# Kernel tuning notes

Measured on AMD Instinct MI355X. Metric: run time of the kernel, lower is better.

## Reference

```python
import jax, jax.numpy as jnp
import numpy as np

DIM = 1024
NUM_HEADS = 16
HEAD_DIM = DIM // NUM_HEADS


def setup_inputs() -> dict:
    key = jax.random.key(0)
    k1, k2, k3, k4, k5 = jax.random.split(key, 5)
    B, N, C = 4, 4096, DIM
    s = 1.0 / np.sqrt(C)
    return {
        "x": jax.random.normal(k1, (B, N, C), dtype=jnp.float32),
        "W_qkv": jax.random.uniform(k2, (C, 3 * C), dtype=jnp.float32, minval=-s, maxval=s),
        "b_qkv": jax.random.uniform(k3, (3 * C,), dtype=jnp.float32, minval=-s, maxval=s),
        "W_proj": jax.random.uniform(k4, (C, C), dtype=jnp.float32, minval=-s, maxval=s),
        "b_proj": jax.random.uniform(k5, (C,), dtype=jnp.float32, minval=-s, maxval=s),
    }


def reference(x, W_qkv, b_qkv, W_proj, b_proj):
    B, N, C = x.shape
    H, D = NUM_HEADS, HEAD_DIM
    qkv = x @ W_qkv + b_qkv                      # [B,N,3C]
    qkv = qkv.reshape(B, N, 3, H, D).transpose(2, 0, 3, 1, 4)  # [3,B,H,N,D]
    q, k, v = qkv[0], qkv[1], qkv[2]
    q = jax.nn.softmax(q, axis=-1)               # softmax over head_dim
    k = jax.nn.softmax(k, axis=-2)               # softmax over sequence N
    context = jnp.einsum('bhnd,bhne->bhde', k, v)  # [B,H,D,D]
    out = jnp.einsum('bhnd,bhde->bhne', q, context)  # [B,H,N,D]
    out = out.transpose(0, 2, 1, 3).reshape(B, N, C)
    return out @ W_proj + b_proj
```

## Files before the change

### kernel.cpp

```cpp
#include <hip/hip_runtime.h>

#define BBATCH 4
#define SEQ 4096
#define CC 1024
#define HH 16
#define DD 64
#define TOKENS 16384
#define QKV3 3072

typedef __attribute__((ext_vector_type(8))) short short8;
typedef __attribute__((ext_vector_type(4))) float floatx4;

__device__ __forceinline__ unsigned short f2bf(float x) {
    unsigned int u = __float_as_uint(x);
    u += 0x7fff + ((u >> 16) & 1);
    return (unsigned short)(u >> 16);
}
__device__ __forceinline__ float bf2f(unsigned short h) {
    return __uint_as_float((unsigned int)h << 16);
}

__device__ __forceinline__ void gload_lds16(const void* g, void* l) {
    __builtin_amdgcn_global_load_lds(
        (const __attribute__((address_space(1))) unsigned int*)g,
        (__attribute__((address_space(3))) unsigned int*)l, 16, 0, 0);
}

__global__ __launch_bounds__(256) void cvt_bf16_kernel(
    const float* __restrict__ X, unsigned short* __restrict__ Y, long n4)
{
    long i = (long)blockIdx.x * 256 + threadIdx.x;
    if (i >= n4) return;
    float4 v = *reinterpret_cast<const float4*>(&X[i * 4]);
    ushort4 h;
    h.x = f2bf(v.x); h.y = f2bf(v.y); h.z = f2bf(v.z); h.w = f2bf(v.w);
    *reinterpret_cast<ushort4*>(&Y[i * 4]) = h;
}

__global__ __launch_bounds__(256) void transpose_bf16_kernel(
    const float* __restrict__ W, int K, int N, unsigned short* __restrict__ T)
{
    __shared__ unsigned short Lh[32][36];
    const int k0 = blockIdx.y * 32, n0 = blockIdx.x * 32;
    const int t = threadIdx.x;
    const int r = t >> 3, c4 = (t & 7) * 4;

    float4 w = *reinterpret_cast<const float4*>(&W[(size_t)(k0 + r) * N + n0 + c4]);
    Lh[r][c4 + 0] = f2bf(w.x);
    Lh[r][c4 + 1] = f2bf(w.y);
    Lh[r][c4 + 2] = f2bf(w.z);
    Lh[r][c4 + 3] = f2bf(w.w);
    __syncthreads();

    const int rn = t >> 3, ck = (t & 7) * 4;
    ushort4 h4;
    h4.x = Lh[ck + 0][rn]; h4.y = Lh[ck + 1][rn];
    h4.z = Lh[ck + 2][rn]; h4.w = Lh[ck + 3][rn];
    *reinterpret_cast<ushort4*>(&T[(size_t)(n0 + rn) * K + k0 + ck]) = h4;
}

template <int MODE>
__global__ __launch_bounds__(512) void gemm256_bf16_kernel(
    const unsigned short* __restrict__ A, int lda,
    const unsigned short* __restrict__ Bt, int ldb,
    const float* __restrict__ bias,
    float* __restrict__ Cf, int ldc,
    unsigned short* __restrict__ Qo, unsigned short* __restrict__ Ko,
    unsigned short* __restrict__ Vo)
{
    __shared__ unsigned short smem[65536];

    const int t = threadIdx.x;
    const int wave = t >> 6, lane = t & 63;

    const int gx = gridDim.x;
    const int nwg = gx * gridDim.y;
    const int id0 = blockIdx.y * gx + blockIdx.x;
    const int cpx = nwg >> 3;
    const int swzid = (id0 & 7) * cpx + (id0 >> 3);
    const int bx = swzid % gx, by = swzid / gx;

    const int row0 = by * 256, col0 = bx * 256;
    const int wave_m = wave >> 2, wave_n = wave & 3;

    const unsigned short* Bp = Bt;
    if (MODE == 0) Bp += ((size_t)(row0 >> 12)) << 20;

    const int fr  = lane & 15;
    const int fqb = (lane >> 4) << 4;
    const int sm  = (fr & 7) << 4;
    const int ck0 = ((0  + fqb) ^ sm) >> 1;
    const int ck1 = ((64 + fqb) ^ sm) >> 1;
    const int aRow = (wave_m * 128 + fr) * 64;
    const int bRow = (wave_n * 64 + fr) * 64;

    int srow[2], scol[2];
#pragma unroll
    for (int e = 0; e < 2; e++) {
        const int P  = (wave << 10) + (lane << 4) + (e << 13);
        const int r  = P >> 7;
        const int pc = P & 127;
        srow[e] = r;
        scol[e] = (pc ^ ((r & 7) << 4)) >> 1;
    }

    auto STAGE_PART = [&](int kt, int buf, int part) {
        const int isB = part >> 1, half = part & 1;
        const unsigned short* p = isB ? Bp : A;
        const int r0 = isB ? col0 : row0;
        const int ld = isB ? ldb : lda;
        const int ldsOff = buf * 32768 + isB * 16384 + half * 8192 + wave * 512;
#pragma unroll
        for (int e = 0; e < 2; e++)
            gload_lds16(&p[(size_t)(r0 + half * 128 + srow[e]) * ld
                           + ((kt & 15) << 6) + scol[e]],
                        &smem[ldsOff + e * 4096]);
    };

    floatx4 acc[8][4];
#pragma unroll
    for (int i = 0; i < 8; i++)
#pragma unroll
        for (int j = 0; j < 4; j++) acc[i][j] = (floatx4)0.0f;

    short8 a[4][2], bl[2][2], bh[2][2];

#define RDA(BUF, IH)                                                          \
    _Pragma("unroll") for (int ii = 0; ii < 4; ii++) {                        \
        a[ii][0] = *reinterpret_cast<const short8*>(                          \
            &smem[(BUF) * 32768 + aRow + ((IH) * 64 + ii * 16) * 64 + ck0]);  \
        a[ii][1] = *reinterpret_cast<const short8*>(                          \
            &smem[(BUF) * 32768 + aRow + ((IH) * 64 + ii * 16) * 64 + ck1]);  \
    }
#define RDB(BUF, JH, DST)                                                     \
    _Pragma("unroll") for (int jj = 0; jj < 2; jj++) {                        \
        DST[jj][0] = *reinterpret_cast<const short8*>(                        \
            &smem[(BUF) * 32768 + 16384 + bRow + ((JH) * 32 + jj * 16) * 64 + ck0]); \
        DST[jj][1] = *reinterpret_cast<const short8*>(                        \
            &smem[(BUF) * 32768 + 16384 + bRow + ((JH) * 32 + jj * 16) * 64 + ck1]); \
    }
#define MFMA_Q(IH, JH, BB)                                                    \
    __builtin_amdgcn_s_setprio(1);                                            \
    _Pragma("unroll") for (int ii = 0; ii < 4; ii++)                          \
    _Pragma("unroll") for (int jj = 0; jj < 2; jj++) {                        \
        acc[(IH)*4+ii][(JH)*2+jj] = __builtin_amdgcn_mfma_f32_16x16x32_bf16(  \
            a[ii][0], BB[jj][0], acc[(IH)*4+ii][(JH)*2+jj], 0, 0, 0);         \
        acc[(IH)*4+ii][(JH)*2+jj] = __builtin_amdgcn_mfma_f32_16x16x32_bf16(  \
            a[ii][1], BB[jj][1], acc[(IH)*4+ii][(JH)*2+jj], 0, 0, 0);         \
    }                                                                         \
    __builtin_amdgcn_s_setprio(0);
#define BARRIER __builtin_amdgcn_s_barrier()
#define WAIT_LGKM asm volatile("s_waitcnt lgkmcnt(0)" ::: "memory")
#define WAIT_VM2  asm volatile("s_waitcnt vmcnt(2)" ::: "memory")

#define KTILE(CUR, OTH, TN, TX)                                               \
    {                                                                         \
        RDA(CUR, 0); RDB(CUR, 0, bl);                                         \
        STAGE_PART(TN, OTH, 1);                                               \
        BARRIER; WAIT_LGKM; MFMA_Q(0, 0, bl); BARRIER;                        \
        RDB(CUR, 1, bh);                                                      \
        STAGE_PART(TN, OTH, 2);                                               \
        BARRIER; WAIT_LGKM; MFMA_Q(0, 1, bh); BARRIER;                        \
        RDA(CUR, 1);                                                          \
        STAGE_PART(TN, OTH, 3);                                               \
        BARRIER; WAIT_LGKM; MFMA_Q(1, 1, bh); BARRIER;                        \
        STAGE_PART(TX, CUR, 0);                                               \
        WAIT_VM2;                                                             \
        BARRIER;                                                              \
        MFMA_Q(1, 0, bl);                                                     \
        BARRIER;                                                              \
    }

    STAGE_PART(0, 0, 0); STAGE_PART(0, 0, 1);
    STAGE_PART(0, 0, 2); STAGE_PART(0, 0, 3);
    STAGE_PART(1, 1, 0);
    WAIT_VM2;
    BARRIER;

#pragma unroll 1
    for (int it = 0; it < 8; it++) {
        const int t1 = 2 * it + 1, t2 = 2 * it + 2, t3 = 2 * it + 3;
        KTILE(0, 1, t1, t2);
        KTILE(1, 0, t2, t3);
    }

#undef KTILE
#undef WAIT_VM2
#undef WAIT_LGKM
#undef BARRIER
#undef MFMA_Q
#undef RDB
#undef RDA

    const int cn = lane & 15, cq = (lane >> 4) * 4;

    if (MODE == 0) {
#pragma unroll
        for (int j = 0; j < 4; j++) {
            const int col = col0 + wave_n * 64 + j * 16 + cn;
            const float bv = bias[col];
#pragma unroll
            for (int i = 0; i < 8; i++)
#pragma unroll
                for (int r = 0; r < 4; r++) {
                    const int row = row0 + wave_m * 128 + i * 16 + cq + r;
                    Cf[(size_t)row * ldc + col] = acc[i][j][r] + bv;
                }
        }
        return;
    }

    __syncthreads();

#pragma unroll
    for (int j = 0; j < 4; j++) {
        const int colL = wave_n * 64 + j * 16 + cn;
        const float bv = bias[col0 + colL];
#pragma unroll
        for (int i = 0; i < 8; i++)
#pragma unroll
            for (int r = 0; r < 4; r++) {
                const int lr = wave_m * 128 + i * 16 + cq + r;
                smem[lr * 256 + (colL ^ ((lr & 7) << 3))] = f2bf(acc[i][j][r] + bv);
            }
    }
    __syncthreads();

    {
        unsigned short* outp = (bx < 4) ? Qo : ((bx < 8) ? Ko : Vo);
        const bool isQ = (bx < 4);
        const int R = t >> 1, half = t & 1;
        const size_t obase = (size_t)(row0 + R) * CC + (col0 & 1023) + half * 128;
        unsigned short* orow = &outp[obase];

#pragma unroll
        for (int g = 0; g < 2; g++) {
            short8 bufv[8];
            const int cbase = half * 16 + g * 8;
#pragma unroll
            for (int k = 0; k < 8; k++)
                bufv[k] = *reinterpret_cast<const short8*>(
                    &smem[R * 256 + (((cbase + k) ^ (R & 7)) << 3)]);
            if (isQ) {
                float v[64];
                float mx = -3.0e38f;
#pragma unroll
                for (int k = 0; k < 8; k++)
#pragma unroll
                    for (int e = 0; e < 8; e++) {
                        const float f = bf2f((unsigned short)bufv[k][e]);
                        v[k * 8 + e] = f;
                        mx = fmaxf(mx, f);
                    }
                float s = 0.0f;
#pragma unroll
                for (int q = 0; q < 64; q++) {
                    const float ev = __expf(v[q] - mx);
                    v[q] = ev;
                    s += ev;
                }
                const float inv = 1.0f / s;
#pragma unroll
                for (int k = 0; k < 8; k++)
#pragma unroll
                    for (int e = 0; e < 8; e++)
                        bufv[k][e] = (short)f2bf(v[k * 8 + e] * inv);
            }
#pragma unroll
            for (int k = 0; k < 8; k++)
                *reinterpret_cast<short8*>(&orow[g * 64 + k * 8]) = bufv[k];
        }
    }
}

__global__ __launch_bounds__(256) void kv_ctx_kernel(
    const unsigned short* __restrict__ Km, const unsigned short* __restrict__ Vm,
    float* __restrict__ ctx_p, float* __restrict__ csum_p)
{
    const int bh = blockIdx.x, ch = blockIdx.y;
    const int b = bh >> 4, h = bh & 15;
    const int t = threadIdx.x;

    __shared__ float Ks[32][68];
    __shared__ float Vs[32][68];
    __shared__ float cred[4][64];

    const int d0 = (t >> 4) * 4, e0 = (t & 15) * 4;
    float acc[4][4];
#pragma unroll
    for (int i = 0; i < 4; i++)
#pragma unroll
        for (int j = 0; j < 4; j++) acc[i][j] = 0.0f;
    float csacc = 0.0f;
    const int dc = t & 63, rq = (t >> 6) * 8;

    const size_t base = (size_t)(b * SEQ + ch * 256) * CC + (size_t)h * 64;

    for (int n0 = 0; n0 < 256; n0 += 32) {
        __syncthreads();
#pragma unroll
        for (int l = 0; l < 2; l++) {
            const int idx = t + l * 256;
            const int r = idx >> 4, c4 = (idx & 15) * 4;
            ushort4 kv = *reinterpret_cast<const ushort4*>(&Km[base + (size_t)(n0 + r) * CC + c4]);
            ushort4 vv = *reinterpret_cast<const ushort4*>(&Vm[base + (size_t)(n0 + r) * CC + c4]);
            float4 kf;
            kf.x = __expf(bf2f(kv.x));
            kf.y = __expf(bf2f(kv.y));
            kf.z = __expf(bf2f(kv.z));
            kf.w = __expf(bf2f(kv.w));
            float4 vf = {bf2f(vv.x), bf2f(vv.y), bf2f(vv.z), bf2f(vv.w)};
            *reinterpret_cast<float4*>(&Ks[r][c4]) = kf;
            *reinterpret_cast<float4*>(&Vs[r][c4]) = vf;
        }
        __syncthreads();

#pragma unroll
        for (int r = 0; r < 8; r++) csacc += Ks[rq + r][dc];

#pragma unroll 8
        for (int n = 0; n < 32; n++) {
            float4 a = *reinterpret_cast<const float4*>(&Ks[n][d0]);
            float4 v4 = *reinterpret_cast<const float4*>(&Vs[n][e0]);
            float a4[4] = {a.x, a.y, a.z, a.w};
            float b4[4] = {v4.x, v4.y, v4.z, v4.w};
#pragma unroll
            for (int i = 0; i < 4; i++)
#pragma unroll
                for (int j = 0; j < 4; j++)
                    acc[i][j] += a4[i] * b4[j];
        }
    }

    __syncthreads();
    cred[t >> 6][dc] = csacc;
    __syncthreads();

    const size_t pslot = (size_t)ch * 64 + bh;
    if (t < 64)
        csum_p[pslot * 64 + t] =
            cred[0][t] + cred[1][t] + cred[2][t] + cred[3][t];

    float* cp = &ctx_p[pslot * 4096];
#pragma unroll
    for (int i = 0; i < 4; i++) {
        float4 v4 = {acc[i][0], acc[i][1], acc[i][2], acc[i][3]};
        *reinterpret_cast<float4*>(&cp[(d0 + i) * 64 + e0]) = v4;
    }
}

__global__ __launch_bounds__(256) void reduce_ctx_kernel(
    const float* __restrict__ ctx_p, const float* __restrict__ csum_p,
    float* __restrict__ ctx, float* __restrict__ csum)
{
    const int bh = blockIdx.x, q = blockIdx.y;
    const int t = threadIdx.x;
#pragma unroll
    for (int e = 0; e < 4; e++) {
        const int idx = (q * 4 + e) * 256 + t;
        float s = 0.0f;
#pragma unroll
        for (int p = 0; p < 16; p++)
            s += ctx_p[((size_t)p * 64 + bh) * 4096 + idx];
        ctx[(size_t)bh * 4096 + idx] = s;
    }
    if (q == 0 && t < 64) {
        float s = 0.0f;
#pragma unroll
        for (int p = 0; p < 16; p++)
            s += csum_p[((size_t)p * 64 + bh) * 64 + t];
        csum[(size_t)bh * 64 + t] = s;
    }
}

__global__ __launch_bounds__(256) void weff_kernel(
    const float* __restrict__ ctx, const float* __restrict__ csum,
    const float* __restrict__ Wp, unsigned short* __restrict__ WeffT)
{
    const int bh = blockIdx.x, nc = blockIdx.y;
    const int b = bh >> 4, h = bh & 15;
    const int t = threadIdx.x;

    __shared__ float ctxs[64 * 64];
    __shared__ float cinvs[64];
#pragma unroll
    for (int l = 0; l < 16; l++)
        ctxs[t + l * 256] = ctx[(size_t)bh * 4096 + t + l * 256];
    if (t < 64) cinvs[t] = 1.0f / csum[(size_t)bh * 64 + t];
    __syncthreads();

    const int n = nc * 128 + (t & 127);
    const int dg = (t >> 7) * 32;

    float acc[32];
#pragma unroll
    for (int d = 0; d < 32; d++) acc[d] = 0.0f;

    for (int e = 0; e < 64; e++) {
        const float w = Wp[(size_t)(h * 64 + e) * CC + n];
#pragma unroll
        for (int d = 0; d < 32; d++)
            acc[d] += ctxs[(dg + d) * 64 + e] * w;
    }

    const size_t obase = ((size_t)b << 20) + (size_t)n * CC + h * 64 + dg;
#pragma unroll
    for (int d = 0; d < 32; d += 2) {
        ushort2 o;
        o.x = f2bf(acc[d] * cinvs[dg + d]);
        o.y = f2bf(acc[d + 1] * cinvs[dg + d + 1]);
        *reinterpret_cast<ushort2*>(&WeffT[obase + d]) = o;
    }
}

extern "C" void kernel_launch(void* const* d_in, const int* in_sizes, int n_in,
                              void* d_out, int out_size, void* d_ws, size_t ws_size,
                              hipStream_t stream)
{
    const float* x      = (const float*)d_in[0];
    const float* W_qkv  = (const float*)d_in[1];
    const float* b_qkv  = (const float*)d_in[2];
    const float* W_proj = (const float*)d_in[3];
    const float* b_proj = (const float*)d_in[4];
    float* out = (float*)d_out;

    unsigned short* Qm  = (unsigned short*)d_ws;
    unsigned short* Km  = Qm + (size_t)TOKENS * CC;
    unsigned short* Vm  = Km + (size_t)TOKENS * CC;
    unsigned short* xb  = Vm + (size_t)TOKENS * CC;
    unsigned short* wqT = xb + (size_t)TOKENS * CC;
    unsigned short* WeffT = wqT + (size_t)QKV3 * CC;
    float* ctx    = (float*)(WeffT + (size_t)BBATCH * CC * CC);
    float* csum   = ctx + (size_t)64 * 4096;
    float* ctx_p  = (float*)xb;
    float* csum_p = ctx_p + (size_t)16 * 64 * 4096;

    cvt_bf16_kernel<<<(TOKENS * CC / 4 + 255) / 256, 256, 0, stream>>>(
        x, xb, (long)TOKENS * CC / 4);
    transpose_bf16_kernel<<<dim3(QKV3 / 32, CC / 32), 256, 0, stream>>>(
        W_qkv, CC, QKV3, wqT);

    gemm256_bf16_kernel<1><<<dim3(QKV3 / 256, TOKENS / 256), 512, 0, stream>>>(
        xb, CC, wqT, CC, b_qkv, (float*)nullptr, 0, Qm, Km, Vm);

    kv_ctx_kernel<<<dim3(BBATCH * HH, 16), 256, 0, stream>>>(Km, Vm, ctx_p, csum_p);

    reduce_ctx_kernel<<<dim3(BBATCH * HH, 4), 256, 0, stream>>>(
        ctx_p, csum_p, ctx, csum);

    weff_kernel<<<dim3(BBATCH * HH, 8), 256, 0, stream>>>(ctx, csum, W_proj, WeffT);

    gemm256_bf16_kernel<0><<<dim3(CC / 256, TOKENS / 256), 512, 0, stream>>>(
        Qm, CC, WeffT, CC, b_proj, out, CC, nullptr, nullptr, nullptr);
}
```

Measured before the change: 371.3 us.

## Split output GEMM into 256x128 tile kernel and retile weff and kv_ctx loads

New measurement: 364.6 us. Within noise of the previous version (-1.8%).

```diff
diff --git a/kernel.cpp b/kernel.cpp
--- a/kernel.cpp
+++ b/kernel.cpp
@@ -59,12 +59,10 @@
     *reinterpret_cast<ushort4*>(&T[(size_t)(n0 + rn) * K + k0 + ck]) = h4;
 }
 
-template <int MODE>
-__global__ __launch_bounds__(512) void gemm256_bf16_kernel(
+__global__ __launch_bounds__(512) void gemm_qkv_kernel(
     const unsigned short* __restrict__ A, int lda,
     const unsigned short* __restrict__ Bt, int ldb,
     const float* __restrict__ bias,
-    float* __restrict__ Cf, int ldc,
     unsigned short* __restrict__ Qo, unsigned short* __restrict__ Ko,
     unsigned short* __restrict__ Vo)
 {
@@ -84,7 +82,6 @@
     const int wave_m = wave >> 2, wave_n = wave & 3;
 
     const unsigned short* Bp = Bt;
-    if (MODE == 0) Bp += ((size_t)(row0 >> 12)) << 20;
 
     const int fr  = lane & 15;
     const int fqb = (lane >> 4) << 4;
@@ -194,22 +191,6 @@
 
     const int cn = lane & 15, cq = (lane >> 4) * 4;
 
-    if (MODE == 0) {
-#pragma unroll
-        for (int j = 0; j < 4; j++) {
-            const int col = col0 + wave_n * 64 + j * 16 + cn;
-            const float bv = bias[col];
-#pragma unroll
-            for (int i = 0; i < 8; i++)
-#pragma unroll
-                for (int r = 0; r < 4; r++) {
-                    const int row = row0 + wave_m * 128 + i * 16 + cq + r;
-                    Cf[(size_t)row * ldc + col] = acc[i][j][r] + bv;
-                }
-        }
-        return;
-    }
-
     __syncthreads();
 
 #pragma unroll
@@ -273,6 +254,146 @@
     }
 }
 
+__global__ __launch_bounds__(512) void gemm_out_kernel(
+    const unsigned short* __restrict__ A, int lda,
+    const unsigned short* __restrict__ Bt, int ldb,
+    const float* __restrict__ bias,
+    float* __restrict__ Cf, int ldc)
+{
+    __shared__ unsigned short smem[49152];
+
+    const int t = threadIdx.x;
+    const int wave = t >> 6, lane = t & 63;
+
+    const int gx = gridDim.x;
+    const int nwg = gx * gridDim.y;
+    const int id0 = blockIdx.y * gx + blockIdx.x;
+    const int cpx = nwg >> 3;
+    const int swzid = (id0 & 7) * cpx + (id0 >> 3);
+    const int bx = swzid % gx, by = swzid / gx;
+
+    const int row0 = by * 256, col0 = bx * 128;
+    const int wave_m = wave >> 2, wave_n = wave & 3;
+
+    const unsigned short* Bp = Bt + (((size_t)(row0 >> 12)) << 20);
+
+    const int fr  = lane & 15;
+    const int fqb = (lane >> 4) << 4;
+    const int sm  = (fr & 7) << 4;
+    const int ck0 = ((0  + fqb) ^ sm) >> 1;
+    const int ck1 = ((64 + fqb) ^ sm) >> 1;
+    const int aRow = (wave_m * 128 + fr) * 64;
+    const int bRow = (wave_n * 32 + fr) * 64;
+
+    int srow[2], scol[2];
+#pragma unroll
+    for (int e = 0; e < 2; e++) {
+        const int P  = (wave << 10) + (lane << 4) + (e << 13);
+        const int r  = P >> 7;
+        const int pc = P & 127;
+        srow[e] = r;
+        scol[e] = (pc ^ ((r & 7) << 4)) >> 1;
+    }
+
+    auto STAGE_PART = [&](int kt, int buf, int part) {
+        const int isB = (part == 2);
+        const unsigned short* p = isB ? Bp : A;
+        const int r0 = isB ? col0 : (row0 + (part & 1) * 128);
+        const int ld = isB ? ldb : lda;
+        const int ldsOff = buf * 24576 + (isB ? 16384 : (part & 1) * 8192) + wave * 512;
+#pragma unroll
+        for (int e = 0; e < 2; e++)
+            gload_lds16(&p[(size_t)(r0 + srow[e]) * ld
+                           + ((kt & 15) << 6) + scol[e]],
+                        &smem[ldsOff + e * 4096]);
+    };
+
+    floatx4 acc[8][2];
+#pragma unroll
+    for (int i = 0; i < 8; i++)
+#pragma unroll
+        for (int j = 0; j < 2; j++) acc[i][j] = (floatx4)0.0f;
+
+    short8 a[4][2], bb[2][2];
+
+#define RDA(BUF, IH)                                                          \
+    _Pragma("unroll") for (int ii = 0; ii < 4; ii++) {                        \
+        a[ii][0] = *reinterpret_cast<const short8*>(                          \
+            &smem[(BUF) * 24576 + aRow + ((IH) * 64 + ii * 16) * 64 + ck0]);  \
+        a[ii][1] = *reinterpret_cast<const short8*>(                          \
+            &smem[(BUF) * 24576 + aRow + ((IH) * 64 + ii * 16) * 64 + ck1]);  \
+    }
+#define RDB(BUF)                                                              \
+    _Pragma("unroll") for (int jj = 0; jj < 2; jj++) {                        \
+        bb[jj][0] = *reinterpret_cast<const short8*>(                         \
+            &smem[(BUF) * 24576 + 16384 + bRow + (jj * 16) * 64 + ck0]);      \
+        bb[jj][1] = *reinterpret_cast<const short8*>(                         \
+            &smem[(BUF) * 24576 + 16384 + bRow + (jj * 16) * 64 + ck1]);      \
+    }
+#define MFMA_8(IH, J)                                                         \
+    __builtin_amdgcn_s_setprio(1);                                            \
+    _Pragma("unroll") for (int ii = 0; ii < 4; ii++) {                        \
+        acc[(IH)*4+ii][(J)] = __builtin_amdgcn_mfma_f32_16x16x32_bf16(        \
+            a[ii][0], bb[(J)][0], acc[(IH)*4+ii][(J)], 0, 0, 0);              \
+        acc[(IH)*4+ii][(J)] = __builtin_amdgcn_mfma_f32_16x16x32_bf16(        \
+            a[ii][1], bb[(J)][1], acc[(IH)*4+ii][(J)], 0, 0, 0);              \
+    }                                                                         \
+    __builtin_amdgcn_s_setprio(0);
+#define BARRIER __builtin_amdgcn_s_barrier()
+#define WAIT_LGKM asm volatile("s_waitcnt lgkmcnt(0)" ::: "memory")
+#define WAIT_VM2  asm volatile("s_waitcnt vmcnt(2)" ::: "memory")
+
+#define KTILE(CUR, OTH, TN, TX)                                               \
+    {                                                                         \
+        RDA(CUR, 0); RDB(CUR);                                                \
+        STAGE_PART(TN, OTH, 1);                                               \
+        BARRIER; WAIT_LGKM; MFMA_8(0, 0); BARRIER;                            \
+        STAGE_PART(TN, OTH, 2);                                               \
+        BARRIER; MFMA_8(0, 1); BARRIER;                                       \
+        RDA(CUR, 1);                                                          \
+        BARRIER; WAIT_LGKM; MFMA_8(1, 1); BARRIER;                            \
+        STAGE_PART(TX, CUR, 0);                                               \
+        WAIT_VM2;                                                             \
+        BARRIER;                                                              \
+        MFMA_8(1, 0);                                                         \
+        BARRIER;                                                              \
+    }
+
+    STAGE_PART(0, 0, 0); STAGE_PART(0, 0, 1); STAGE_PART(0, 0, 2);
+    STAGE_PART(1, 1, 0);
+    WAIT_VM2;
+    BARRIER;
+
+#pragma unroll 1
+    for (int it = 0; it < 8; it++) {
+        const int t1 = 2 * it + 1, t2 = 2 * it + 2, t3 = 2 * it + 3;
+        KTILE(0, 1, t1, t2);
+        KTILE(1, 0, t2, t3);
+    }
+
+#undef KTILE
+#undef WAIT_VM2
+#undef WAIT_LGKM
+#undef BARRIER
+#undef MFMA_8
+#undef RDB
+#undef RDA
+
+    const int cn = lane & 15, cq = (lane >> 4) * 4;
+#pragma unroll
+    for (int j = 0; j < 2; j++) {
+        const int col = col0 + wave_n * 32 + j * 16 + cn;
+        const float bv = bias[col];
+#pragma unroll
+        for (int i = 0; i < 8; i++)
+#pragma unroll
+            for (int r = 0; r < 4; r++) {
+                const int row = row0 + wave_m * 128 + i * 16 + cq + r;
+                Cf[(size_t)row * ldc + col] = acc[i][j][r] + bv;
+            }
+    }
+}
+
 __global__ __launch_bounds__(256) void kv_ctx_kernel(
     const unsigned short* __restrict__ Km, const unsigned short* __restrict__ Vm,
     float* __restrict__ ctx_p, float* __restrict__ csum_p)
@@ -295,23 +416,30 @@
     const int dc = t & 63, rq = (t >> 6) * 8;
 
     const size_t base = (size_t)(b * SEQ + ch * 256) * CC + (size_t)h * 64;
+    const int lr = t >> 3, lc = (t & 7) * 8;
 
     for (int n0 = 0; n0 < 256; n0 += 32) {
         __syncthreads();
-#pragma unroll
-        for (int l = 0; l < 2; l++) {
-            const int idx = t + l * 256;
-            const int r = idx >> 4, c4 = (idx & 15) * 4;
-            ushort4 kv = *reinterpret_cast<const ushort4*>(&Km[base + (size_t)(n0 + r) * CC + c4]);
-            ushort4 vv = *reinterpret_cast<const ushort4*>(&Vm[base + (size_t)(n0 + r) * CC + c4]);
-            float4 kf;
-            kf.x = __expf(bf2f(kv.x));
-            kf.y = __expf(bf2f(kv.y));
-            kf.z = __expf(bf2f(kv.z));
-            kf.w = __expf(bf2f(kv.w));
-            float4 vf = {bf2f(vv.x), bf2f(vv.y), bf2f(vv.z), bf2f(vv.w)};
-            *reinterpret_cast<float4*>(&Ks[r][c4]) = kf;
-            *reinterpret_cast<float4*>(&Vs[r][c4]) = vf;
+        {
+            short8 k8 = *reinterpret_cast<const short8*>(&Km[base + (size_t)(n0 + lr) * CC + lc]);
+            short8 v8 = *reinterpret_cast<const short8*>(&Vm[base + (size_t)(n0 + lr) * CC + lc]);
+            float4 ka, kb, va, vb;
+            ka.x = __expf(bf2f((unsigned short)k8[0]));
+            ka.y = __expf(bf2f((unsigned short)k8[1]));
+            ka.z = __expf(bf2f((unsigned short)k8[2]));
+            ka.w = __expf(bf2f((unsigned short)k8[3]));
+            kb.x = __expf(bf2f((unsigned short)k8[4]));
+            kb.y = __expf(bf2f((unsigned short)k8[5]));
+            kb.z = __expf(bf2f((unsigned short)k8[6]));
+            kb.w = __expf(bf2f((unsigned short)k8[7]));
+            va.x = bf2f((unsigned short)v8[0]); va.y = bf2f((unsigned short)v8[1]);
+            va.z = bf2f((unsigned short)v8[2]); va.w = bf2f((unsigned short)v8[3]);
+            vb.x = bf2f((unsigned short)v8[4]); vb.y = bf2f((unsigned short)v8[5]);
+            vb.z = bf2f((unsigned short)v8[6]); vb.w = bf2f((unsigned short)v8[7]);
+            *reinterpret_cast<float4*>(&Ks[lr][lc])     = ka;
+            *reinterpret_cast<float4*>(&Ks[lr][lc + 4]) = kb;
+            *reinterpret_cast<float4*>(&Vs[lr][lc])     = va;
+            *reinterpret_cast<float4*>(&Vs[lr][lc + 4]) = vb;
         }
         __syncthreads();
 
@@ -344,7 +472,8 @@
     float* cp = &ctx_p[pslot * 4096];
 #pragma unroll
     for (int i = 0; i < 4; i++) {
-        float4 v4 = {acc[i][0], acc[i][1], acc[i][2], acc[i][3]};
+        float4 v4;
+        v4.x = acc[i][0]; v4.y = acc[i][1]; v4.z = acc[i][2]; v4.w = acc[i][3];
         *reinterpret_cast<float4*>(&cp[(d0 + i) * 64 + e0]) = v4;
     }
 }
@@ -381,35 +510,54 @@
     const int b = bh >> 4, h = bh & 15;
     const int t = threadIdx.x;
 
-    __shared__ float ctxs[64 * 64];
+    __shared__ float ctxsT[64 * 68];
+    __shared__ float WpS[64 * 128];
     __shared__ float cinvs[64];
-#pragma unroll
-    for (int l = 0; l < 16; l++)
-        ctxs[t + l * 256] = ctx[(size_t)bh * 4096 + t + l * 256];
+
+#pragma unroll
+    for (int l = 0; l < 16; l++) {
+        const int idx = t + l * 256;
+        ctxsT[(idx & 63) * 68 + (idx >> 6)] = ctx[(size_t)bh * 4096 + idx];
+    }
+#pragma unroll
+    for (int l = 0; l < 32; l++) {
+        const int idx = t + l * 256;
+        WpS[idx] = Wp[(size_t)(h * 64 + (idx >> 7)) * CC + nc * 128 + (idx & 127)];
+    }
     if (t < 64) cinvs[t] = 1.0f / csum[(size_t)bh * 64 + t];
     __syncthreads();
 
-    const int n = nc * 128 + (t & 127);
-    const int dg = (t >> 7) * 32;
-
-    float acc[32];
-#pragma unroll
-    for (int d = 0; d < 32; d++) acc[d] = 0.0f;
-
+    const int d0 = (t >> 5) * 8;
+    const int n0 = (t & 31) * 4;
+
+    float acc[8][4];
+#pragma unroll
+    for (int i = 0; i < 8; i++)
+#pragma unroll
+        for (int j = 0; j < 4; j++) acc[i][j] = 0.0f;
+
+#pragma unroll 4
     for (int e = 0; e < 64; e++) {
-        const float w = Wp[(size_t)(h * 64 + e) * CC + n];
-#pragma unroll
-        for (int d = 0; d < 32; d++)
-            acc[d] += ctxs[(dg + d) * 64 + e] * w;
-    }
-
-    const size_t obase = ((size_t)b << 20) + (size_t)n * CC + h * 64 + dg;
-#pragma unroll
-    for (int d = 0; d < 32; d += 2) {
-        ushort2 o;
-        o.x = f2bf(acc[d] * cinvs[dg + d]);
-        o.y = f2bf(acc[d + 1] * cinvs[dg + d + 1]);
-        *reinterpret_cast<ushort2*>(&WeffT[obase + d]) = o;
+        float4 c0 = *reinterpret_cast<const float4*>(&ctxsT[e * 68 + d0]);
+        float4 c1 = *reinterpret_cast<const float4*>(&ctxsT[e * 68 + d0 + 4]);
+        float4 w4 = *reinterpret_cast<const float4*>(&WpS[e * 128 + n0]);
+        const float cc[8] = {c0.x, c0.y, c0.z, c0.w, c1.x, c1.y, c1.z, c1.w};
+        const float ww[4] = {w4.x, w4.y, w4.z, w4.w};
+#pragma unroll
+        for (int i = 0; i < 8; i++)
+#pragma unroll
+            for (int j = 0; j < 4; j++)
+                acc[i][j] += cc[i] * ww[j];
+    }
+
+    const size_t obase = ((size_t)b << 20) + (size_t)(nc * 128 + n0) * CC + h * 64 + d0;
+#pragma unroll
+    for (int j = 0; j < 4; j++) {
+        short8 o;
+#pragma unroll
+        for (int i = 0; i < 8; i++)
+            o[i] = (short)f2bf(acc[i][j] * cinvs[d0 + i]);
+        *reinterpret_cast<short8*>(&WeffT[obase + (size_t)j * CC]) = o;
     }
 }
 
@@ -440,8 +588,8 @@
     transpose_bf16_kernel<<<dim3(QKV3 / 32, CC / 32), 256, 0, stream>>>(
         W_qkv, CC, QKV3, wqT);
 
-    gemm256_bf16_kernel<1><<<dim3(QKV3 / 256, TOKENS / 256), 512, 0, stream>>>(
-        xb, CC, wqT, CC, b_qkv, (float*)nullptr, 0, Qm, Km, Vm);
+    gemm_qkv_kernel<<<dim3(QKV3 / 256, TOKENS / 256), 512, 0, stream>>>(
+        xb, CC, wqT, CC, b_qkv, Qm, Km, Vm);
 
     kv_ctx_kernel<<<dim3(BBATCH * HH, 16), 256, 0, stream>>>(Km, Vm, ctx_p, csum_p);
 
@@ -450,6 +598,6 @@
 
     weff_kernel<<<dim3(BBATCH * HH, 8), 256, 0, stream>>>(ctx, csum, W_proj, WeffT);
 
-    gemm256_bf16_kernel<0><<<dim3(CC / 256, TOKENS / 256), 512, 0, stream>>>(
-        Qm, CC, WeffT, CC, b_proj, out, CC, nullptr, nullptr, nullptr);
-}
+    gemm_out_kernel<<<dim3(CC / 128, TOKENS / 256), 512, 0, stream>>>(
+        Qm, CC, WeffT, CC, b_proj, out, CC);
+}
```
